# Kernel optimization log

Hardware: AMD Instinct MI355X
Metric: run time of the kernel (lower is better)

Reference implementation:

```python
import jax, jax.numpy as jnp
import numpy as np

T, B = 1024, 16384
GAMMA = 0.99
LAMBDA = 0.97


def setup_inputs() -> dict:
    key = jax.random.key(0)
    k1, k2 = jax.random.split(key)
    value = jax.random.normal(k1, (T + 1, B), dtype=jnp.float32)
    reward = jax.random.normal(k2, (T, B), dtype=jnp.float32)
    return {"value": value, "reward": reward}


def reference(value, reward):
    # delta[t] = r[t] + gamma * V[t+1] - V[t]          shape (T, B)
    delta = reward + GAMMA * value[1:] - value[:-1]
    coef = jnp.float32(GAMMA * LAMBDA)

    def step(carry, d):
        adv_t = d + coef * carry
        return adv_t, adv_t

    init = jnp.zeros(delta.shape[1:], dtype=delta.dtype)
    # reverse-in-time scan: adv[t] = delta[t] + gamma*lambda * adv[t+1]
    _, adv = jax.lax.scan(step, init, delta, reverse=True)
    return adv
```

## Files before the change

### kernel.cpp

```cpp
#include <hip/hip_runtime.h>


constexpr int T_ = 1024;
constexpr int B_ = 16384;
constexpr int L_ = 16;
constexpr int C_ = T_ / L_;
constexpr float GAMMA = 0.99f;
constexpr float COEF  = (float)(0.99 * 0.97);

__host__ __device__ constexpr float pow_coef(int n) {
    float p = 1.0f;
    for (int i = 0; i < n; ++i) p *= COEF;
    return p;
}
constexpr float CL = pow_coef(L_);

__global__ __launch_bounds__(256) void gae_local(
    const float* __restrict__ value,
    const float* __restrict__ reward,
    float* __restrict__ S,
    float* __restrict__ out)
{
    const int c4    = blockIdx.x * 256 + threadIdx.x;
    const int chunk = blockIdx.y;
    const size_t b  = (size_t)c4 * 4;
    const int t0    = chunk * L_;

    float4 v[L_ + 1];
    float4 r[L_];
    #pragma unroll
    for (int i = 0; i <= L_; ++i)
        v[i] = *(const float4*)(value + (size_t)(t0 + i) * B_ + b);
    #pragma unroll
    for (int i = 0; i < L_; ++i)
        r[i] = *(const float4*)(reward + (size_t)(t0 + i) * B_ + b);

    float4 a = make_float4(0.f, 0.f, 0.f, 0.f);
    #pragma unroll
    for (int i = L_ - 1; i >= 0; --i) {
        a.x = (r[i].x + GAMMA * v[i + 1].x - v[i].x) + COEF * a.x;
        a.y = (r[i].y + GAMMA * v[i + 1].y - v[i].y) + COEF * a.y;
        a.z = (r[i].z + GAMMA * v[i + 1].z - v[i].z) + COEF * a.z;
        a.w = (r[i].w + GAMMA * v[i + 1].w - v[i].w) + COEF * a.w;
        *(float4*)(out + (size_t)(t0 + i) * B_ + b) = a;
    }
    *(float4*)(S + (size_t)chunk * B_ + b) = a;
}

__global__ __launch_bounds__(256) void gae_carry(float* __restrict__ S)
{
    const int col = blockIdx.x * 256 + threadIdx.x;

    float s[C_];
    #pragma unroll
    for (int j = 0; j < C_; ++j)
        s[j] = S[(size_t)j * B_ + col];

    float run = 0.f;
    #pragma unroll
    for (int j = C_ - 1; j >= 0; --j) {
        S[(size_t)j * B_ + col] = run;
        run = s[j] + CL * run;
    }
}

__global__ __launch_bounds__(256) void gae_fix(
    const float* __restrict__ S,
    float* __restrict__ out)
{
    const int c4    = blockIdx.x * 256 + threadIdx.x;
    const int chunk = blockIdx.y;
    const size_t b  = (size_t)c4 * 4;
    const int t0    = chunk * L_;

    float4 carry = *(const float4*)(S + (size_t)chunk * B_ + b);

    float4 o[L_];
    #pragma unroll
    for (int i = 0; i < L_; ++i)
        o[i] = *(const float4*)(out + (size_t)(t0 + i) * B_ + b);

    float p = COEF;
    #pragma unroll
    for (int i = L_ - 1; i >= 0; --i) {
        o[i].x += p * carry.x;
        o[i].y += p * carry.y;
        o[i].z += p * carry.z;
        o[i].w += p * carry.w;
        *(float4*)(out + (size_t)(t0 + i) * B_ + b) = o[i];
        p *= COEF;
    }
}

extern "C" void kernel_launch(void* const* d_in, const int* in_sizes, int n_in,
                              void* d_out, int out_size, void* d_ws, size_t ws_size,
                              hipStream_t stream) {
    const float* value  = (const float*)d_in[0];
    const float* reward = (const float*)d_in[1];
    float* out = (float*)d_out;
    float* S   = (float*)d_ws;

    dim3 block(256);
    dim3 gridA(B_ / 4 / 256, C_);
    dim3 gridC(B_ / 256);
    dim3 gridF(B_ / 4 / 256, C_ - 1);

    gae_local<<<gridA, block, 0, stream>>>(value, reward, S, out);
    gae_carry<<<gridC, block, 0, stream>>>(S);
    gae_fix  <<<gridF, block, 0, stream>>>(S, out);
}
```

Baseline: 189.9 us.

## Replace local-scan+fix passes with reduce-then-rescan using carry-in seeding

The first pass now only computes per-chunk partial sums without writing the output. The final pass recomputes the chunk scan from value and reward, seeded with the propagated carry, and writes the output once. This removes the read-modify-write of the full output array, at the cost of rereading the inputs. Chunk length is templated and drops to 8 when the workspace allows, doubling the number of chunks the serial carry kernel walks. Occupancy hints are added to the launch bounds.

```diff
diff --git a/kernel.cpp b/kernel.cpp
--- a/kernel.cpp
+++ b/kernel.cpp
@@ -3,8 +3,6 @@
 
 constexpr int T_ = 1024;
 constexpr int B_ = 16384;
-constexpr int L_ = 16;
-constexpr int C_ = T_ / L_;
 constexpr float GAMMA = 0.99f;
 constexpr float COEF  = (float)(0.99 * 0.97);
 
@@ -13,83 +11,102 @@
     for (int i = 0; i < n; ++i) p *= COEF;
     return p;
 }
-constexpr float CL = pow_coef(L_);
 
-__global__ __launch_bounds__(256) void gae_local(
+template <int L>
+__global__ __launch_bounds__(256, 4) void gae_sum(
     const float* __restrict__ value,
     const float* __restrict__ reward,
-    float* __restrict__ S,
+    float* __restrict__ S)
+{
+    const int c4    = blockIdx.x * 256 + threadIdx.x;
+    const int chunk = blockIdx.y;
+    const size_t b  = (size_t)c4 * 4;
+    const int t0    = chunk * L;
+
+    float4 v[L + 1];
+    float4 r[L];
+    #pragma unroll
+    for (int i = 0; i <= L; ++i)
+        v[i] = *(const float4*)(value + (size_t)(t0 + i) * B_ + b);
+    #pragma unroll
+    for (int i = 0; i < L; ++i)
+        r[i] = *(const float4*)(reward + (size_t)(t0 + i) * B_ + b);
+
+    float4 s = make_float4(0.f, 0.f, 0.f, 0.f);
+    #pragma unroll
+    for (int i = L - 1; i >= 0; --i) {
+        s.x = (r[i].x + GAMMA * v[i + 1].x - v[i].x) + COEF * s.x;
+        s.y = (r[i].y + GAMMA * v[i + 1].y - v[i].y) + COEF * s.y;
+        s.z = (r[i].z + GAMMA * v[i + 1].z - v[i].z) + COEF * s.z;
+        s.w = (r[i].w + GAMMA * v[i + 1].w - v[i].w) + COEF * s.w;
+    }
+    *(float4*)(S + (size_t)chunk * B_ + b) = s;
+}
+
+template <int L>
+__global__ __launch_bounds__(256, 1) void gae_carry(float* __restrict__ S)
+{
+    constexpr int C  = T_ / L;
+    constexpr float CL = pow_coef(L);
+    const int col = blockIdx.x * 256 + threadIdx.x;
+
+    float s[C];
+    #pragma unroll
+    for (int j = 0; j < C; ++j)
+        s[j] = S[(size_t)j * B_ + col];
+
+    float run = 0.f;
+    #pragma unroll
+    for (int j = C - 1; j >= 0; --j) {
+        S[(size_t)j * B_ + col] = run;
+        run = s[j] + CL * run;
+    }
+}
+
+template <int L>
+__global__ __launch_bounds__(256, 4) void gae_emit(
+    const float* __restrict__ value,
+    const float* __restrict__ reward,
+    const float* __restrict__ S,
     float* __restrict__ out)
 {
     const int c4    = blockIdx.x * 256 + threadIdx.x;
     const int chunk = blockIdx.y;
     const size_t b  = (size_t)c4 * 4;
-    const int t0    = chunk * L_;
+    const int t0    = chunk * L;
 
-    float4 v[L_ + 1];
-    float4 r[L_];
+    float4 carry = *(const float4*)(S + (size_t)chunk * B_ + b);
+
+    float4 v[L + 1];
+    float4 r[L];
     #pragma unroll
-    for (int i = 0; i <= L_; ++i)
+    for (int i = 0; i <= L; ++i)
         v[i] = *(const float4*)(value + (size_t)(t0 + i) * B_ + b);
     #pragma unroll
-    for (int i = 0; i < L_; ++i)
+    for (int i = 0; i < L; ++i)
         r[i] = *(const float4*)(reward + (size_t)(t0 + i) * B_ + b);
 
-    float4 a = make_float4(0.f, 0.f, 0.f, 0.f);
+    float4 a = carry;
     #pragma unroll
-    for (int i = L_ - 1; i >= 0; --i) {
+    for (int i = L - 1; i >= 0; --i) {
         a.x = (r[i].x + GAMMA * v[i + 1].x - v[i].x) + COEF * a.x;
         a.y = (r[i].y + GAMMA * v[i + 1].y - v[i].y) + COEF * a.y;
         a.z = (r[i].z + GAMMA * v[i + 1].z - v[i].z) + COEF * a.z;
         a.w = (r[i].w + GAMMA * v[i + 1].w - v[i].w) + COEF * a.w;
         *(float4*)(out + (size_t)(t0 + i) * B_ + b) = a;
     }
-    *(float4*)(S + (size_t)chunk * B_ + b) = a;
 }
 
-__global__ __launch_bounds__(256) void gae_carry(float* __restrict__ S)
-{
-    const int col = blockIdx.x * 256 + threadIdx.x;
-
-    float s[C_];
-    #pragma unroll
-    for (int j = 0; j < C_; ++j)
-        s[j] = S[(size_t)j * B_ + col];
-
-    float run = 0.f;
-    #pragma unroll
-    for (int j = C_ - 1; j >= 0; --j) {
-        S[(size_t)j * B_ + col] = run;
-        run = s[j] + CL * run;
-    }
-}
-
-__global__ __launch_bounds__(256) void gae_fix(
-    const float* __restrict__ S,
-    float* __restrict__ out)
-{
-    const int c4    = blockIdx.x * 256 + threadIdx.x;
-    const int chunk = blockIdx.y;
-    const size_t b  = (size_t)c4 * 4;
-    const int t0    = chunk * L_;
-
-    float4 carry = *(const float4*)(S + (size_t)chunk * B_ + b);
-
-    float4 o[L_];
-    #pragma unroll
-    for (int i = 0; i < L_; ++i)
-        o[i] = *(const float4*)(out + (size_t)(t0 + i) * B_ + b);
-
-    float p = COEF;
-    #pragma unroll
-    for (int i = L_ - 1; i >= 0; --i) {
-        o[i].x += p * carry.x;
-        o[i].y += p * carry.y;
-        o[i].z += p * carry.z;
-        o[i].w += p * carry.w;
-        *(float4*)(out + (size_t)(t0 + i) * B_ + b) = o[i];
-        p *= COEF;
-    }
+template <int L>
+static void launch_all(const float* value, const float* reward,
+                       float* S, float* out, hipStream_t stream) {
+    constexpr int C = T_ / L;
+    dim3 block(256);
+    dim3 gridA(B_ / 4 / 256, C);
+    dim3 gridC(B_ / 256);
+    gae_sum<L>  <<<gridA, block, 0, stream>>>(value, reward, S);
+    gae_carry<L><<<gridC, block, 0, stream>>>(S);
+    gae_emit<L> <<<gridA, block, 0, stream>>>(value, reward, S, out);
 }
 
 extern "C" void kernel_launch(void* const* d_in, const int* in_sizes, int n_in,
@@ -100,12 +117,9 @@
     float* out = (float*)d_out;
     float* S   = (float*)d_ws;
 
-    dim3 block(256);
-    dim3 gridA(B_ / 4 / 256, C_);
-    dim3 gridC(B_ / 256);
-    dim3 gridF(B_ / 4 / 256, C_ - 1);
-
-    gae_local<<<gridA, block, 0, stream>>>(value, reward, S, out);
-    gae_carry<<<gridC, block, 0, stream>>>(S);
-    gae_fix  <<<gridF, block, 0, stream>>>(S, out);
+    if (ws_size >= (size_t)(T_ / 8) * B_ * 4) {
+        launch_all<8>(value, reward, S, out, stream);
+    } else {
+        launch_all<16>(value, reward, S, out, stream);
+    }
 }
```

Measured after the change: 194.7 us. 2.5% more time.
